# Performance work log

Hardware: AMD Instinct MI355X
Metric: run time of the kernel (lower is better)

## Reference

```python
import jax, jax.numpy as jnp
import numpy as np


def _graph_conv_mean(x, src, dst, edge_weight, W_rel, W_root, b, num_nodes):
    # messages: gather source features, optionally scale by edge weight
    msg = x[src]  # [E, D]
    if edge_weight is not None:
        msg = msg * edge_weight[:, None]
    # mean aggregation over incoming edges per destination node
    summed = jax.ops.segment_sum(msg, dst, num_segments=num_nodes)  # [N, D]
    count = jax.ops.segment_sum(jnp.ones((src.shape[0],), x.dtype), dst, num_segments=num_nodes)
    mean = summed / jnp.maximum(count, 1.0)[:, None]
    # out = lin_rel(mean) + lin_root(x) + bias
    return mean @ W_rel + x @ W_root + b


def setup_inputs() -> dict:
    key = jax.random.key(0)
    ks = jax.random.split(key, 8)
    N, E, D, H, C = 100000, 1600000, 128, 32, 5
    x = jax.random.normal(ks[0], (N, D), dtype=jnp.float32)
    edge_index = jax.random.randint(ks[1], (2, E), 0, N, dtype=jnp.int64)
    edge_weight = jax.random.uniform(ks[2], (E,), dtype=jnp.float32)
    W_rel1 = jax.random.normal(ks[3], (D, H), dtype=jnp.float32) / np.sqrt(D)
    W_root1 = jax.random.normal(ks[4], (D, H), dtype=jnp.float32) / np.sqrt(D)
    b1 = jnp.zeros((H,), jnp.float32)
    W_rel2 = jax.random.normal(ks[5], (H, C), dtype=jnp.float32) / np.sqrt(H)
    W_root2 = jax.random.normal(ks[6], (H, C), dtype=jnp.float32) / np.sqrt(H)
    b2 = jnp.zeros((C,), jnp.float32)
    return {"x": x, "edge_index": edge_index, "edge_weight": edge_weight,
            "W_rel1": W_rel1, "W_root1": W_root1, "b1": b1,
            "W_rel2": W_rel2, "W_root2": W_root2, "b2": b2}


def reference(x, edge_index, edge_weight, W_rel1, W_root1, b1, W_rel2, W_root2, b2):
    N = x.shape[0]
    src, dst = edge_index[0], edge_index[1]
    # conv1 with edge_weight
    h = _graph_conv_mean(x, src, dst, edge_weight, W_rel1, W_root1, b1, N)
    h = jax.nn.relu(h)
    # dropout is identity at inference (training=False)
    # conv2 without edge_weight
    out = _graph_conv_mean(h, src, dst, None, W_rel2, W_root2, b2, N)
    return jax.nn.log_softmax(out, axis=1)
```

## Files before the change

### kernel.cpp

```cpp
#include <hip/hip_runtime.h>
#include <math.h>

#define N_NODES 100000
#define E_EDGES 1600000
#define D_IN    128
#define H_MID   32
#define C_OUT   5

#define BSHIFT 9
#define BNODES 512
#define NBKT   196
#define BCAP   9200
#define SRC_BITS 17
#define SRC_MASK 0x1FFFF

#define KP 136

typedef __attribute__((ext_vector_type(8))) short bf16x8;
typedef __attribute__((ext_vector_type(4))) float f32x4;

__device__ inline unsigned f2bf(float f) {
    unsigned u = __float_as_uint(f);
    return (u + 0x7FFFu + ((u >> 16) & 1u)) >> 16;
}

__global__ void k_prep(const float* __restrict__ Wrel,
                       const float* __restrict__ Wroot,
                       int* __restrict__ bucket_cursor,
                       unsigned short* __restrict__ wt_g) {
    int tid = threadIdx.x;
    bucket_cursor[tid] = 0;
    for (int i = tid; i < 64 * 128; i += 256) {
        int n = i >> 7, k = i & 127;
        float v = (n < H_MID) ? Wrel[k * H_MID + n] : Wroot[k * H_MID + (n - H_MID)];
        wt_g[i] = (unsigned short)f2bf(v);
    }
}

__global__ __launch_bounds__(256) void k1_mfma(
    const float* __restrict__ x,
    const unsigned short* __restrict__ wt_g,
    const float* __restrict__ b1,
    unsigned short* __restrict__ xrelh,
    float* __restrict__ xroot) {
    __shared__ unsigned short xs[64 * KP];
    int tid = threadIdx.x;
    int nodeBase = blockIdx.x * 64;

    #pragma unroll
    for (int it = 0; it < 16; ++it) {
        int idx = it * 256 + tid;
        int row = idx >> 6, kp = idx & 63;
        int node = nodeBase + row;
        float2 v = make_float2(0.f, 0.f);
        if (node < N_NODES)
            v = *(const float2*)(x + (size_t)node * D_IN + kp * 2);
        unsigned pk = f2bf(v.x) | (f2bf(v.y) << 16);
        *(unsigned*)(xs + row * KP + kp * 2) = pk;
    }
    __syncthreads();

    int lane = tid & 63;
    int wv = tid >> 6;
    int m = lane & 15;
    int quad = lane >> 4;

    f32x4 acc[4];
    #pragma unroll
    for (int nt = 0; nt < 4; ++nt) acc[nt] = (f32x4){0.f, 0.f, 0.f, 0.f};

    #pragma unroll
    for (int kk = 0; kk < 4; ++kk) {
        int k0 = kk * 32 + quad * 8;
        bf16x8 a = *(const bf16x8*)(xs + (wv * 16 + m) * KP + k0);
        #pragma unroll
        for (int nt = 0; nt < 4; ++nt) {
            bf16x8 b = *(const bf16x8*)(wt_g + (nt * 16 + m) * 128 + k0);
            acc[nt] = __builtin_amdgcn_mfma_f32_16x16x32_bf16(a, b, acc[nt], 0, 0, 0);
        }
    }

    #pragma unroll
    for (int nt = 0; nt < 4; ++nt) {
        #pragma unroll
        for (int r = 0; r < 4; ++r) {
            int node = nodeBase + wv * 16 + quad * 4 + r;
            int colg = nt * 16 + m;
            if (node < N_NODES) {
                if (colg < H_MID) {
                    xrelh[(size_t)node * H_MID + colg] =
                        (unsigned short)f2bf(acc[nt][r]);
                } else {
                    int c = colg - H_MID;
                    xroot[(size_t)node * H_MID + c] = acc[nt][r] + b1[c];
                }
            }
        }
    }
}

__global__ __launch_bounds__(1024) void k_binA(
    const int* __restrict__ src,
    const int* __restrict__ dst,
    const float* __restrict__ ew,
    int* __restrict__ bucket_cursor,
    int2* __restrict__ staged) {
    __shared__ int cnt[NBKT];
    __shared__ int lstart[NBKT];
    __shared__ int gbase[NBKT];
    __shared__ int scanbuf[256];
    __shared__ int2 ebuf[2048];
    __shared__ short bbuf[2048];
    int tid = threadIdx.x;
    int eBase = blockIdx.x * 2048;

    if (tid < NBKT) cnt[tid] = 0;
    __syncthreads();

    int b[2], rank[2], packed[2], wbits[2];
    bool valid[2];
    #pragma unroll
    for (int u = 0; u < 2; ++u) {
        int e = eBase + u * 1024 + tid;
        valid[u] = (e < E_EDGES);
        b[u] = 0; rank[u] = 0; packed[u] = 0; wbits[u] = 0;
        if (valid[u]) {
            int d = dst[e];
            int s = src[e];
            wbits[u] = __float_as_int(ew[e]);
            b[u] = d >> BSHIFT;
            packed[u] = ((d & (BNODES - 1)) << SRC_BITS) | s;
            rank[u] = atomicAdd(&cnt[b[u]], 1);
        }
    }
    __syncthreads();

    if (tid < 256) scanbuf[tid] = (tid < NBKT) ? cnt[tid] : 0;
    __syncthreads();
    for (int off = 1; off < 256; off <<= 1) {
        int t = 0;
        if (tid < 256 && tid >= off) t = scanbuf[tid - off];
        __syncthreads();
        if (tid < 256) scanbuf[tid] += t;
        __syncthreads();
    }
    if (tid < NBKT) {
        lstart[tid] = scanbuf[tid] - cnt[tid];
        gbase[tid]  = atomicAdd(&bucket_cursor[tid], cnt[tid]);
    }
    __syncthreads();
    int total = scanbuf[NBKT - 1];

    #pragma unroll
    for (int u = 0; u < 2; ++u) {
        if (valid[u]) {
            int slot = lstart[b[u]] + rank[u];
            ebuf[slot] = make_int2(packed[u], wbits[u]);
            bbuf[slot] = (short)b[u];
        }
    }
    __syncthreads();

    for (int t = tid; t < total; t += 1024) {
        int2 ev = ebuf[t];
        int bb = bbuf[t];
        int gpos = gbase[bb] + (t - lstart[bb]);
        if (gpos < BCAP)
            staged[(size_t)bb * BCAP + gpos] = ev;
    }
}

__global__ __launch_bounds__(1024) void k_binB2(
    const int* __restrict__ bucket_cursor,
    const int2* __restrict__ staged,
    int* __restrict__ deg,
    int* __restrict__ offsets,
    int2* __restrict__ csr8) {
    __shared__ int hist[BNODES];
    __shared__ int scanb[BNODES];
    __shared__ int cur[BNODES];
    __shared__ int sbase[256];
    int tid = threadIdx.x;
    int b = blockIdx.x;

    if (tid < 256) {
        int c = (tid < NBKT) ? bucket_cursor[tid] : 0;
        sbase[tid] = (c > BCAP) ? BCAP : c;
    }
    if (tid < BNODES) hist[tid] = 0;
    __syncthreads();
    for (int off = 1; off < 256; off <<= 1) {
        int t = 0;
        if (tid < 256 && tid >= off) t = sbase[tid - off];
        __syncthreads();
        if (tid < 256) sbase[tid] += t;
        __syncthreads();
    }
    int count = bucket_cursor[b];
    if (count > BCAP) count = BCAP;
    int base = sbase[b] - count;
    int nodeBase = b << BSHIFT;
    const int2* sp = staged + (size_t)b * BCAP;

    for (int i = tid; i < count; i += 1024)
        atomicAdd(&hist[((unsigned)sp[i].x) >> SRC_BITS], 1);
    __syncthreads();

    int v = 0;
    if (tid < BNODES) {
        v = hist[tid];
        scanb[tid] = v;
    }
    __syncthreads();
    for (int off = 1; off < BNODES; off <<= 1) {
        int t = 0;
        if (tid < BNODES && tid >= off) t = scanb[tid - off];
        __syncthreads();
        if (tid < BNODES) scanb[tid] += t;
        __syncthreads();
    }
    if (tid < BNODES) {
        int excl = scanb[tid] - v;
        int node = nodeBase + tid;
        if (node < N_NODES) {
            deg[node]     = v;
            offsets[node] = base + excl;
        }
        cur[tid] = excl;
    }
    __syncthreads();

    for (int i = tid; i < count; i += 1024) {
        int2 ev = sp[i];
        int local = ((unsigned)ev.x) >> SRC_BITS;
        int pos = atomicAdd(&cur[local], 1);
        csr8[base + pos] = make_int2(ev.x & SRC_MASK, ev.y);
    }
}

__global__ __launch_bounds__(512) void k_layer1(
    const int* __restrict__ offsets,
    const int* __restrict__ deg,
    const int2* __restrict__ csr8,
    const unsigned short* __restrict__ xrelh,
    const float* __restrict__ xroot,
    const float* __restrict__ Wrel2,
    const float* __restrict__ Wroot2,
    const float* __restrict__ b2,
    float* __restrict__ h2rel,
    float* __restrict__ h2root) {
    int node = blockIdx.x * 32 + (threadIdx.x >> 4);
    int lane = threadIdx.x & 15;
    int beg = offsets[node];
    int dg  = deg[node];
    int end = beg + dg;

    float acc0 = 0.f, acc1 = 0.f;
    int i = beg;
    for (; i + 8 <= end; i += 8) {
        int2 e[8];
        unsigned v[8];
        #pragma unroll
        for (int u = 0; u < 8; ++u) e[u] = csr8[i + u];
        #pragma unroll
        for (int u = 0; u < 8; ++u)
            v[u] = *(const unsigned*)(xrelh + (size_t)e[u].x * H_MID + lane * 2);
        #pragma unroll
        for (int u = 0; u < 8; ++u) {
            float w = __int_as_float(e[u].y);
            acc0 += __uint_as_float((v[u] & 0xFFFFu) << 16) * w;
            acc1 += __uint_as_float(v[u] & 0xFFFF0000u) * w;
        }
    }
    for (; i < end; ++i) {
        int2 e0 = csr8[i];
        unsigned v0 = *(const unsigned*)(xrelh + (size_t)e0.x * H_MID + lane * 2);
        float w0 = __int_as_float(e0.y);
        acc0 += __uint_as_float((v0 & 0xFFFFu) << 16) * w0;
        acc1 += __uint_as_float(v0 & 0xFFFF0000u) * w0;
    }

    float inv = 1.0f / fmaxf((float)dg, 1.0f);
    float2 rt = *(const float2*)(xroot + (size_t)node * H_MID + lane * 2);
    float h0 = fmaxf(acc0 * inv + rt.x, 0.f);
    float h1 = fmaxf(acc1 * inv + rt.y, 0.f);

    float p[2 * C_OUT];
    #pragma unroll
    for (int j = 0; j < C_OUT; ++j) {
        p[j]         = h0 * Wrel2[(2 * lane) * C_OUT + j]
                     + h1 * Wrel2[(2 * lane + 1) * C_OUT + j];
        p[C_OUT + j] = h0 * Wroot2[(2 * lane) * C_OUT + j]
                     + h1 * Wroot2[(2 * lane + 1) * C_OUT + j];
    }
    #pragma unroll
    for (int mm = 8; mm > 0; mm >>= 1) {
        #pragma unroll
        for (int j = 0; j < 2 * C_OUT; ++j)
            p[j] += __shfl_xor(p[j], mm, 16);
    }
    if (lane == 0) {
        #pragma unroll
        for (int j = 0; j < C_OUT; ++j) {
            h2rel[(size_t)node * C_OUT + j]  = p[j];
            h2root[(size_t)node * C_OUT + j] = p[C_OUT + j] + b2[j];
        }
    }
}

__global__ __launch_bounds__(256) void k_layer2(
    const int* __restrict__ offsets,
    const int* __restrict__ deg,
    const int2* __restrict__ csr8,
    const float* __restrict__ h2rel,
    const float* __restrict__ h2root,
    float* __restrict__ out) {
    int node = blockIdx.x * 32 + (threadIdx.x >> 3);
    int lane = threadIdx.x & 7;
    int beg = offsets[node];
    int dg  = deg[node];
    int end = beg + dg;

    float acc = 0.f;
    if (lane < C_OUT) {
        int i = beg;
        for (; i + 8 <= end; i += 8) {
            int s[8];
            float v[8];
            #pragma unroll
            for (int u = 0; u < 8; ++u) s[u] = csr8[i + u].x;
            #pragma unroll
            for (int u = 0; u < 8; ++u)
                v[u] = h2rel[(size_t)s[u] * C_OUT + lane];
            #pragma unroll
            for (int u = 0; u < 8; ++u) acc += v[u];
        }
        for (; i < end; ++i)
            acc += h2rel[(size_t)csr8[i].x * C_OUT + lane];
    }
    float inv = 1.0f / fmaxf((float)dg, 1.0f);
    float o = (lane < C_OUT)
                  ? acc * inv + h2root[(size_t)node * C_OUT + lane]
                  : -INFINITY;
    float m = o;
    #pragma unroll
    for (int dd = 4; dd > 0; dd >>= 1) m = fmaxf(m, __shfl_xor(m, dd, 8));
    float e = (lane < C_OUT) ? expf(o - m) : 0.f;
    float ssum = e;
    #pragma unroll
    for (int dd = 4; dd > 0; dd >>= 1) ssum += __shfl_xor(ssum, dd, 8);
    float lse = m + logf(ssum);
    if (lane < C_OUT)
        out[(size_t)node * C_OUT + lane] = o - lse;
}

extern "C" void kernel_launch(void* const* d_in, const int* in_sizes, int n_in,
                              void* d_out, int out_size, void* d_ws, size_t ws_size,
                              hipStream_t stream) {
    const float* x      = (const float*)d_in[0];
    const int*   ei     = (const int*)d_in[1];
    const float* ew     = (const float*)d_in[2];
    const float* Wrel1  = (const float*)d_in[3];
    const float* Wroot1 = (const float*)d_in[4];
    const float* b1     = (const float*)d_in[5];
    const float* Wrel2  = (const float*)d_in[6];
    const float* Wroot2 = (const float*)d_in[7];
    const float* b2     = (const float*)d_in[8];
    float* out = (float*)d_out;

    const int* src = ei;
    const int* dst = ei + E_EDGES;

    char* ws = (char*)d_ws;
    int*   deg           = (int*)ws;
    int*   bucket_cursor = deg + N_NODES;
    unsigned short* wt_g = (unsigned short*)(bucket_cursor + 256);
    int*   offsets       = (int*)(wt_g + 64 * 128);
    int2*  csr8          = (int2*)(offsets + N_NODES);
    unsigned short* xrelh = (unsigned short*)(csr8 + E_EDGES);
    float* xroot         = (float*)(xrelh + (size_t)N_NODES * H_MID);
    float* h2rel         = xroot + (size_t)N_NODES * H_MID;
    float* h2root        = h2rel + (size_t)N_NODES * C_OUT;
    int2*  staged        = (int2*)xrelh;

    k_prep<<<1, 256, 0, stream>>>(Wrel1, Wroot1, bucket_cursor, wt_g);

    k_binA<<<(E_EDGES + 2047) / 2048, 1024, 0, stream>>>(src, dst, ew,
                                                         bucket_cursor, staged);
    k_binB2<<<NBKT, 1024, 0, stream>>>(bucket_cursor, staged,
                                       deg, offsets, csr8);

    k1_mfma<<<(N_NODES + 63) / 64, 256, 0, stream>>>(x, wt_g, b1,
                                                     xrelh, xroot);

    k_layer1<<<N_NODES / 32, 512, 0, stream>>>(offsets, deg, csr8,
                                               xrelh, xroot, Wrel2, Wroot2, b2,
                                               h2rel, h2root);

    k_layer2<<<N_NODES / 32, 256, 0, stream>>>(offsets, deg, csr8,
                                               h2rel, h2root, out);
}
```

Before: 224.3 us.

## Split CSR into separate src/weight arrays, smaller buckets, prefetch edge indices in aggregation

```diff
diff --git a/kernel.cpp b/kernel.cpp
--- a/kernel.cpp
+++ b/kernel.cpp
@@ -7,10 +7,10 @@
 #define H_MID   32
 #define C_OUT   5
 
-#define BSHIFT 9
-#define BNODES 512
-#define NBKT   196
-#define BCAP   9200
+#define BSHIFT 8
+#define BNODES 256
+#define NBKT   391
+#define BCAP   4800
 #define SRC_BITS 17
 #define SRC_MASK 0x1FFFF
 
@@ -30,7 +30,7 @@
                        unsigned short* __restrict__ wt_g) {
     int tid = threadIdx.x;
     bucket_cursor[tid] = 0;
-    for (int i = tid; i < 64 * 128; i += 256) {
+    for (int i = tid; i < 64 * 128; i += 512) {
         int n = i >> 7, k = i & 127;
         float v = (n < H_MID) ? Wrel[k * H_MID + n] : Wroot[k * H_MID + (n - H_MID)];
         wt_g[i] = (unsigned short)f2bf(v);
@@ -108,7 +108,7 @@
     __shared__ int cnt[NBKT];
     __shared__ int lstart[NBKT];
     __shared__ int gbase[NBKT];
-    __shared__ int scanbuf[256];
+    __shared__ int scanbuf[512];
     __shared__ int2 ebuf[2048];
     __shared__ short bbuf[2048];
     int tid = threadIdx.x;
@@ -135,13 +135,13 @@
     }
     __syncthreads();
 
-    if (tid < 256) scanbuf[tid] = (tid < NBKT) ? cnt[tid] : 0;
-    __syncthreads();
-    for (int off = 1; off < 256; off <<= 1) {
+    if (tid < 512) scanbuf[tid] = (tid < NBKT) ? cnt[tid] : 0;
+    __syncthreads();
+    for (int off = 1; off < 512; off <<= 1) {
         int t = 0;
-        if (tid < 256 && tid >= off) t = scanbuf[tid - off];
-        __syncthreads();
-        if (tid < 256) scanbuf[tid] += t;
+        if (tid < 512 && tid >= off) t = scanbuf[tid - off];
+        __syncthreads();
+        if (tid < 512) scanbuf[tid] += t;
         __syncthreads();
     }
     if (tid < NBKT) {
@@ -175,25 +175,26 @@
     const int2* __restrict__ staged,
     int* __restrict__ deg,
     int* __restrict__ offsets,
-    int2* __restrict__ csr8) {
+    int* __restrict__ csr_src,
+    int* __restrict__ csr_wi) {
     __shared__ int hist[BNODES];
     __shared__ int scanb[BNODES];
     __shared__ int cur[BNODES];
-    __shared__ int sbase[256];
+    __shared__ int sbase[512];
     int tid = threadIdx.x;
     int b = blockIdx.x;
 
-    if (tid < 256) {
+    if (tid < 512) {
         int c = (tid < NBKT) ? bucket_cursor[tid] : 0;
         sbase[tid] = (c > BCAP) ? BCAP : c;
     }
     if (tid < BNODES) hist[tid] = 0;
     __syncthreads();
-    for (int off = 1; off < 256; off <<= 1) {
+    for (int off = 1; off < 512; off <<= 1) {
         int t = 0;
-        if (tid < 256 && tid >= off) t = sbase[tid - off];
-        __syncthreads();
-        if (tid < 256) sbase[tid] += t;
+        if (tid < 512 && tid >= off) t = sbase[tid - off];
+        __syncthreads();
+        if (tid < 512) sbase[tid] += t;
         __syncthreads();
     }
     int count = bucket_cursor[b];
@@ -233,15 +234,17 @@
     for (int i = tid; i < count; i += 1024) {
         int2 ev = sp[i];
         int local = ((unsigned)ev.x) >> SRC_BITS;
-        int pos = atomicAdd(&cur[local], 1);
-        csr8[base + pos] = make_int2(ev.x & SRC_MASK, ev.y);
-    }
-}
-
-__global__ __launch_bounds__(512) void k_layer1(
+        int pos = base + atomicAdd(&cur[local], 1);
+        csr_src[pos] = ev.x & SRC_MASK;
+        csr_wi[pos]  = ev.y;
+    }
+}
+
+__global__ __launch_bounds__(256) void k_layer1(
     const int* __restrict__ offsets,
     const int* __restrict__ deg,
-    const int2* __restrict__ csr8,
+    const int* __restrict__ csr_src,
+    const float* __restrict__ csr_w,
     const unsigned short* __restrict__ xrelh,
     const float* __restrict__ xroot,
     const float* __restrict__ Wrel2,
@@ -249,7 +252,7 @@
     const float* __restrict__ b2,
     float* __restrict__ h2rel,
     float* __restrict__ h2root) {
-    int node = blockIdx.x * 32 + (threadIdx.x >> 4);
+    int node = blockIdx.x * 16 + (threadIdx.x >> 4);
     int lane = threadIdx.x & 15;
     int beg = offsets[node];
     int dg  = deg[node];
@@ -257,25 +260,43 @@
 
     float acc0 = 0.f, acc1 = 0.f;
     int i = beg;
-    for (; i + 8 <= end; i += 8) {
-        int2 e[8];
+    int nfull = dg >> 3;
+    if (nfull) {
+        int s[8]; float w[8];
+        #pragma unroll
+        for (int u = 0; u < 8; ++u) { s[u] = csr_src[i + u]; w[u] = csr_w[i + u]; }
+        for (int bb = 1; bb < nfull; ++bb) {
+            unsigned v[8];
+            #pragma unroll
+            for (int u = 0; u < 8; ++u)
+                v[u] = *(const unsigned*)(xrelh + (size_t)s[u] * H_MID + lane * 2);
+            int s2[8]; float w2[8];
+            #pragma unroll
+            for (int u = 0; u < 8; ++u) { s2[u] = csr_src[i + 8 + u]; w2[u] = csr_w[i + 8 + u]; }
+            #pragma unroll
+            for (int u = 0; u < 8; ++u) {
+                acc0 += __uint_as_float((v[u] & 0xFFFFu) << 16) * w[u];
+                acc1 += __uint_as_float(v[u] & 0xFFFF0000u) * w[u];
+            }
+            #pragma unroll
+            for (int u = 0; u < 8; ++u) { s[u] = s2[u]; w[u] = w2[u]; }
+            i += 8;
+        }
         unsigned v[8];
         #pragma unroll
-        for (int u = 0; u < 8; ++u) e[u] = csr8[i + u];
-        #pragma unroll
         for (int u = 0; u < 8; ++u)
-            v[u] = *(const unsigned*)(xrelh + (size_t)e[u].x * H_MID + lane * 2);
+            v[u] = *(const unsigned*)(xrelh + (size_t)s[u] * H_MID + lane * 2);
         #pragma unroll
         for (int u = 0; u < 8; ++u) {
-            float w = __int_as_float(e[u].y);
-            acc0 += __uint_as_float((v[u] & 0xFFFFu) << 16) * w;
-            acc1 += __uint_as_float(v[u] & 0xFFFF0000u) * w;
-        }
+            acc0 += __uint_as_float((v[u] & 0xFFFFu) << 16) * w[u];
+            acc1 += __uint_as_float(v[u] & 0xFFFF0000u) * w[u];
+        }
+        i += 8;
     }
     for (; i < end; ++i) {
-        int2 e0 = csr8[i];
-        unsigned v0 = *(const unsigned*)(xrelh + (size_t)e0.x * H_MID + lane * 2);
-        float w0 = __int_as_float(e0.y);
+        int s0 = csr_src[i];
+        float w0 = csr_w[i];
+        unsigned v0 = *(const unsigned*)(xrelh + (size_t)s0 * H_MID + lane * 2);
         acc0 += __uint_as_float((v0 & 0xFFFFu) << 16) * w0;
         acc1 += __uint_as_float(v0 & 0xFFFF0000u) * w0;
     }
@@ -311,7 +332,7 @@
 __global__ __launch_bounds__(256) void k_layer2(
     const int* __restrict__ offsets,
     const int* __restrict__ deg,
-    const int2* __restrict__ csr8,
+    const int* __restrict__ csr_src,
     const float* __restrict__ h2rel,
     const float* __restrict__ h2root,
     float* __restrict__ out) {
@@ -324,19 +345,32 @@
     float acc = 0.f;
     if (lane < C_OUT) {
         int i = beg;
-        for (; i + 8 <= end; i += 8) {
+        int nfull = dg >> 3;
+        if (nfull) {
             int s[8];
-            float v[8];
-            #pragma unroll
-            for (int u = 0; u < 8; ++u) s[u] = csr8[i + u].x;
+            #pragma unroll
+            for (int u = 0; u < 8; ++u) s[u] = csr_src[i + u];
+            for (int bb = 1; bb < nfull; ++bb) {
+                float v[8];
+                #pragma unroll
+                for (int u = 0; u < 8; ++u)
+                    v[u] = h2rel[(size_t)s[u] * C_OUT + lane];
+                int s2[8];
+                #pragma unroll
+                for (int u = 0; u < 8; ++u) s2[u] = csr_src[i + 8 + u];
+                #pragma unroll
+                for (int u = 0; u < 8; ++u) acc += v[u];
+                #pragma unroll
+                for (int u = 0; u < 8; ++u) s[u] = s2[u];
+                i += 8;
+            }
             #pragma unroll
             for (int u = 0; u < 8; ++u)
-                v[u] = h2rel[(size_t)s[u] * C_OUT + lane];
-            #pragma unroll
-            for (int u = 0; u < 8; ++u) acc += v[u];
+                acc += h2rel[(size_t)s[u] * C_OUT + lane];
+            i += 8;
         }
         for (; i < end; ++i)
-            acc += h2rel[(size_t)csr8[i].x * C_OUT + lane];
+            acc += h2rel[(size_t)csr_src[i] * C_OUT + lane];
     }
     float inv = 1.0f / fmaxf((float)dg, 1.0f);
     float o = (lane < C_OUT)
@@ -374,29 +408,31 @@
     char* ws = (char*)d_ws;
     int*   deg           = (int*)ws;
     int*   bucket_cursor = deg + N_NODES;
-    unsigned short* wt_g = (unsigned short*)(bucket_cursor + 256);
+    unsigned short* wt_g = (unsigned short*)(bucket_cursor + 512);
     int*   offsets       = (int*)(wt_g + 64 * 128);
-    int2*  csr8          = (int2*)(offsets + N_NODES);
-    unsigned short* xrelh = (unsigned short*)(csr8 + E_EDGES);
+    int*   csr_src       = offsets + N_NODES;
+    int*   csr_wi        = csr_src + E_EDGES;
+    unsigned short* xrelh = (unsigned short*)(csr_wi + E_EDGES);
     float* xroot         = (float*)(xrelh + (size_t)N_NODES * H_MID);
     float* h2rel         = xroot + (size_t)N_NODES * H_MID;
     float* h2root        = h2rel + (size_t)N_NODES * C_OUT;
     int2*  staged        = (int2*)xrelh;
 
-    k_prep<<<1, 256, 0, stream>>>(Wrel1, Wroot1, bucket_cursor, wt_g);
+    k_prep<<<1, 512, 0, stream>>>(Wrel1, Wroot1, bucket_cursor, wt_g);
 
     k_binA<<<(E_EDGES + 2047) / 2048, 1024, 0, stream>>>(src, dst, ew,
                                                          bucket_cursor, staged);
     k_binB2<<<NBKT, 1024, 0, stream>>>(bucket_cursor, staged,
-                                       deg, offsets, csr8);
+                                       deg, offsets, csr_src, csr_wi);
 
     k1_mfma<<<(N_NODES + 63) / 64, 256, 0, stream>>>(x, wt_g, b1,
                                                      xrelh, xroot);
 
-    k_layer1<<<N_NODES / 32, 512, 0, stream>>>(offsets, deg, csr8,
+    k_layer1<<<N_NODES / 16, 256, 0, stream>>>(offsets, deg, csr_src,
+                                               (const float*)csr_wi,
                                                xrelh, xroot, Wrel2, Wroot2, b2,
                                                h2rel, h2root);
 
-    k_layer2<<<N_NODES / 32, 256, 0, stream>>>(offsets, deg, csr8,
+    k_layer2<<<N_NODES / 32, 256, 0, stream>>>(offsets, deg, csr_src,
                                                h2rel, h2root, out);
 }
```

Measured after the change: 227.1 us. Within noise of the previous version (+1.2%).

## Drop CSR build; aggregate directly from bucketed edges with LDS atomics

Applied to the files above, without the earlier changes.

```diff
diff --git a/kernel.cpp b/kernel.cpp
--- a/kernel.cpp
+++ b/kernel.cpp
@@ -7,14 +7,16 @@
 #define H_MID   32
 #define C_OUT   5
 
-#define BSHIFT 9
-#define BNODES 512
-#define NBKT   196
-#define BCAP   9200
+#define BSHIFT 8
+#define BNODES 256
+#define NBKT   391
+#define BCAP   4500
 #define SRC_BITS 17
 #define SRC_MASK 0x1FFFF
-
-#define KP 136
+#define EB     4096
+
+#define KP   136
+#define ACCP 33
 
 typedef __attribute__((ext_vector_type(8))) short bf16x8;
 typedef __attribute__((ext_vector_type(4))) float f32x4;
@@ -23,6 +25,9 @@
     unsigned u = __float_as_uint(f);
     return (u + 0x7FFFu + ((u >> 16) & 1u)) >> 16;
 }
+
+__device__ inline float bflo(unsigned v) { return __uint_as_float((v & 0xFFFFu) << 16); }
+__device__ inline float bfhi(unsigned v) { return __uint_as_float(v & 0xFFFF0000u); }
 
 __global__ void k_prep(const float* __restrict__ Wrel,
                        const float* __restrict__ Wroot,
@@ -30,7 +35,7 @@
                        unsigned short* __restrict__ wt_g) {
     int tid = threadIdx.x;
     bucket_cursor[tid] = 0;
-    for (int i = tid; i < 64 * 128; i += 256) {
+    for (int i = tid; i < 64 * 128; i += 512) {
         int n = i >> 7, k = i & 127;
         float v = (n < H_MID) ? Wrel[k * H_MID + n] : Wroot[k * H_MID + (n - H_MID)];
         wt_g[i] = (unsigned short)f2bf(v);
@@ -108,19 +113,19 @@
     __shared__ int cnt[NBKT];
     __shared__ int lstart[NBKT];
     __shared__ int gbase[NBKT];
-    __shared__ int scanbuf[256];
-    __shared__ int2 ebuf[2048];
-    __shared__ short bbuf[2048];
+    __shared__ int scanbuf[512];
+    __shared__ int2 ebuf[EB];
+    __shared__ short bbuf[EB];
     int tid = threadIdx.x;
-    int eBase = blockIdx.x * 2048;
+    int eBase = blockIdx.x * EB;
 
     if (tid < NBKT) cnt[tid] = 0;
     __syncthreads();
 
-    int b[2], rank[2], packed[2], wbits[2];
-    bool valid[2];
-    #pragma unroll
-    for (int u = 0; u < 2; ++u) {
+    int b[4], rank[4], packed[4], wbits[4];
+    bool valid[4];
+    #pragma unroll
+    for (int u = 0; u < 4; ++u) {
         int e = eBase + u * 1024 + tid;
         valid[u] = (e < E_EDGES);
         b[u] = 0; rank[u] = 0; packed[u] = 0; wbits[u] = 0;
@@ -135,13 +140,13 @@
     }
     __syncthreads();
 
-    if (tid < 256) scanbuf[tid] = (tid < NBKT) ? cnt[tid] : 0;
-    __syncthreads();
-    for (int off = 1; off < 256; off <<= 1) {
+    if (tid < 512) scanbuf[tid] = (tid < NBKT) ? cnt[tid] : 0;
+    __syncthreads();
+    for (int off = 1; off < 512; off <<= 1) {
         int t = 0;
-        if (tid < 256 && tid >= off) t = scanbuf[tid - off];
+        if (tid < 512 && tid >= off) t = scanbuf[tid - off];
         __syncthreads();
-        if (tid < 256) scanbuf[tid] += t;
+        if (tid < 512) scanbuf[tid] += t;
         __syncthreads();
     }
     if (tid < NBKT) {
@@ -152,7 +157,7 @@
     int total = scanbuf[NBKT - 1];
 
     #pragma unroll
-    for (int u = 0; u < 2; ++u) {
+    for (int u = 0; u < 4; ++u) {
         if (valid[u]) {
             int slot = lstart[b[u]] + rank[u];
             ebuf[slot] = make_int2(packed[u], wbits[u]);
@@ -170,78 +175,9 @@
     }
 }
 
-__global__ __launch_bounds__(1024) void k_binB2(
+__global__ __launch_bounds__(1024) void k_layer1B(
     const int* __restrict__ bucket_cursor,
     const int2* __restrict__ staged,
-    int* __restrict__ deg,
-    int* __restrict__ offsets,
-    int2* __restrict__ csr8) {
-    __shared__ int hist[BNODES];
-    __shared__ int scanb[BNODES];
-    __shared__ int cur[BNODES];
-    __shared__ int sbase[256];
-    int tid = threadIdx.x;
-    int b = blockIdx.x;
-
-    if (tid < 256) {
-        int c = (tid < NBKT) ? bucket_cursor[tid] : 0;
-        sbase[tid] = (c > BCAP) ? BCAP : c;
-    }
-    if (tid < BNODES) hist[tid] = 0;
-    __syncthreads();
-    for (int off = 1; off < 256; off <<= 1) {
-        int t = 0;
-        if (tid < 256 && tid >= off) t = sbase[tid - off];
-        __syncthreads();
-        if (tid < 256) sbase[tid] += t;
-        __syncthreads();
-    }
-    int count = bucket_cursor[b];
-    if (count > BCAP) count = BCAP;
-    int base = sbase[b] - count;
-    int nodeBase = b << BSHIFT;
-    const int2* sp = staged + (size_t)b * BCAP;
-
-    for (int i = tid; i < count; i += 1024)
-        atomicAdd(&hist[((unsigned)sp[i].x) >> SRC_BITS], 1);
-    __syncthreads();
-
-    int v = 0;
-    if (tid < BNODES) {
-        v = hist[tid];
-        scanb[tid] = v;
-    }
-    __syncthreads();
-    for (int off = 1; off < BNODES; off <<= 1) {
-        int t = 0;
-        if (tid < BNODES && tid >= off) t = scanb[tid - off];
-        __syncthreads();
-        if (tid < BNODES) scanb[tid] += t;
-        __syncthreads();
-    }
-    if (tid < BNODES) {
-        int excl = scanb[tid] - v;
-        int node = nodeBase + tid;
-        if (node < N_NODES) {
-            deg[node]     = v;
-            offsets[node] = base + excl;
-        }
-        cur[tid] = excl;
-    }
-    __syncthreads();
-
-    for (int i = tid; i < count; i += 1024) {
-        int2 ev = sp[i];
-        int local = ((unsigned)ev.x) >> SRC_BITS;
-        int pos = atomicAdd(&cur[local], 1);
-        csr8[base + pos] = make_int2(ev.x & SRC_MASK, ev.y);
-    }
-}
-
-__global__ __launch_bounds__(512) void k_layer1(
-    const int* __restrict__ offsets,
-    const int* __restrict__ deg,
-    const int2* __restrict__ csr8,
     const unsigned short* __restrict__ xrelh,
     const float* __restrict__ xroot,
     const float* __restrict__ Wrel2,
@@ -249,109 +185,182 @@
     const float* __restrict__ b2,
     float* __restrict__ h2rel,
     float* __restrict__ h2root) {
-    int node = blockIdx.x * 32 + (threadIdx.x >> 4);
-    int lane = threadIdx.x & 15;
-    int beg = offsets[node];
-    int dg  = deg[node];
-    int end = beg + dg;
-
-    float acc0 = 0.f, acc1 = 0.f;
-    int i = beg;
-    for (; i + 8 <= end; i += 8) {
-        int2 e[8];
-        unsigned v[8];
-        #pragma unroll
-        for (int u = 0; u < 8; ++u) e[u] = csr8[i + u];
-        #pragma unroll
-        for (int u = 0; u < 8; ++u)
-            v[u] = *(const unsigned*)(xrelh + (size_t)e[u].x * H_MID + lane * 2);
-        #pragma unroll
-        for (int u = 0; u < 8; ++u) {
-            float w = __int_as_float(e[u].y);
-            acc0 += __uint_as_float((v[u] & 0xFFFFu) << 16) * w;
-            acc1 += __uint_as_float(v[u] & 0xFFFF0000u) * w;
-        }
-    }
-    for (; i < end; ++i) {
-        int2 e0 = csr8[i];
-        unsigned v0 = *(const unsigned*)(xrelh + (size_t)e0.x * H_MID + lane * 2);
+    __shared__ float acc[BNODES * ACCP];
+    __shared__ int hist[BNODES];
+    int tid = threadIdx.x;
+    int b = blockIdx.x;
+
+    for (int i = tid; i < BNODES * ACCP; i += 1024) acc[i] = 0.f;
+    if (tid < BNODES) hist[tid] = 0;
+    __syncthreads();
+
+    int count = bucket_cursor[b];
+    if (count > BCAP) count = BCAP;
+    const int2* sp = staged + (size_t)b * BCAP;
+
+    int g = tid >> 4;
+    int lane = tid & 15;
+
+    int nb = count >> 8;
+    for (int r = 0; r < nb; ++r) {
+        int i = (r << 8) + (g << 2);
+        int2 e0 = sp[i], e1 = sp[i + 1], e2 = sp[i + 2], e3 = sp[i + 3];
+        unsigned v0 = *(const unsigned*)(xrelh + (size_t)(e0.x & SRC_MASK) * H_MID + lane * 2);
+        unsigned v1 = *(const unsigned*)(xrelh + (size_t)(e1.x & SRC_MASK) * H_MID + lane * 2);
+        unsigned v2 = *(const unsigned*)(xrelh + (size_t)(e2.x & SRC_MASK) * H_MID + lane * 2);
+        unsigned v3 = *(const unsigned*)(xrelh + (size_t)(e3.x & SRC_MASK) * H_MID + lane * 2);
+        int d0 = ((unsigned)e0.x) >> SRC_BITS;
+        int d1 = ((unsigned)e1.x) >> SRC_BITS;
+        int d2 = ((unsigned)e2.x) >> SRC_BITS;
+        int d3 = ((unsigned)e3.x) >> SRC_BITS;
         float w0 = __int_as_float(e0.y);
-        acc0 += __uint_as_float((v0 & 0xFFFFu) << 16) * w0;
-        acc1 += __uint_as_float(v0 & 0xFFFF0000u) * w0;
-    }
-
-    float inv = 1.0f / fmaxf((float)dg, 1.0f);
-    float2 rt = *(const float2*)(xroot + (size_t)node * H_MID + lane * 2);
-    float h0 = fmaxf(acc0 * inv + rt.x, 0.f);
-    float h1 = fmaxf(acc1 * inv + rt.y, 0.f);
-
-    float p[2 * C_OUT];
-    #pragma unroll
-    for (int j = 0; j < C_OUT; ++j) {
-        p[j]         = h0 * Wrel2[(2 * lane) * C_OUT + j]
-                     + h1 * Wrel2[(2 * lane + 1) * C_OUT + j];
-        p[C_OUT + j] = h0 * Wroot2[(2 * lane) * C_OUT + j]
-                     + h1 * Wroot2[(2 * lane + 1) * C_OUT + j];
-    }
-    #pragma unroll
-    for (int mm = 8; mm > 0; mm >>= 1) {
-        #pragma unroll
-        for (int j = 0; j < 2 * C_OUT; ++j)
-            p[j] += __shfl_xor(p[j], mm, 16);
-    }
-    if (lane == 0) {
-        #pragma unroll
-        for (int j = 0; j < C_OUT; ++j) {
-            h2rel[(size_t)node * C_OUT + j]  = p[j];
-            h2root[(size_t)node * C_OUT + j] = p[C_OUT + j] + b2[j];
-        }
-    }
-}
-
-__global__ __launch_bounds__(256) void k_layer2(
-    const int* __restrict__ offsets,
-    const int* __restrict__ deg,
-    const int2* __restrict__ csr8,
+        float w1 = __int_as_float(e1.y);
+        float w2 = __int_as_float(e2.y);
+        float w3 = __int_as_float(e3.y);
+        atomicAdd(&acc[d0 * ACCP + 2 * lane],     bflo(v0) * w0);
+        atomicAdd(&acc[d0 * ACCP + 2 * lane + 1], bfhi(v0) * w0);
+        atomicAdd(&acc[d1 * ACCP + 2 * lane],     bflo(v1) * w1);
+        atomicAdd(&acc[d1 * ACCP + 2 * lane + 1], bfhi(v1) * w1);
+        atomicAdd(&acc[d2 * ACCP + 2 * lane],     bflo(v2) * w2);
+        atomicAdd(&acc[d2 * ACCP + 2 * lane + 1], bfhi(v2) * w2);
+        atomicAdd(&acc[d3 * ACCP + 2 * lane],     bflo(v3) * w3);
+        atomicAdd(&acc[d3 * ACCP + 2 * lane + 1], bfhi(v3) * w3);
+        if (lane == 0) {
+            atomicAdd(&hist[d0], 1);
+            atomicAdd(&hist[d1], 1);
+            atomicAdd(&hist[d2], 1);
+            atomicAdd(&hist[d3], 1);
+        }
+    }
+    for (int i = (nb << 8) + g; i < count; i += 64) {
+        int2 e0 = sp[i];
+        unsigned v0 = *(const unsigned*)(xrelh + (size_t)(e0.x & SRC_MASK) * H_MID + lane * 2);
+        int d0 = ((unsigned)e0.x) >> SRC_BITS;
+        float w0 = __int_as_float(e0.y);
+        atomicAdd(&acc[d0 * ACCP + 2 * lane],     bflo(v0) * w0);
+        atomicAdd(&acc[d0 * ACCP + 2 * lane + 1], bfhi(v0) * w0);
+        if (lane == 0) atomicAdd(&hist[d0], 1);
+    }
+    __syncthreads();
+
+    #pragma unroll
+    for (int pass = 0; pass < 4; ++pass) {
+        int nl = pass * 64 + (tid >> 4);
+        int node = b * BNODES + nl;
+        if (node < N_NODES) {
+            int dg = hist[nl];
+            float inv = 1.0f / fmaxf((float)dg, 1.0f);
+            float a0 = acc[nl * ACCP + 2 * lane] * inv;
+            float a1 = acc[nl * ACCP + 2 * lane + 1] * inv;
+            float2 rt = *(const float2*)(xroot + (size_t)node * H_MID + lane * 2);
+            float h0 = fmaxf(a0 + rt.x, 0.f);
+            float h1 = fmaxf(a1 + rt.y, 0.f);
+
+            float p[2 * C_OUT];
+            #pragma unroll
+            for (int j = 0; j < C_OUT; ++j) {
+                p[j]         = h0 * Wrel2[(2 * lane) * C_OUT + j]
+                             + h1 * Wrel2[(2 * lane + 1) * C_OUT + j];
+                p[C_OUT + j] = h0 * Wroot2[(2 * lane) * C_OUT + j]
+                             + h1 * Wroot2[(2 * lane + 1) * C_OUT + j];
+            }
+            #pragma unroll
+            for (int mm = 8; mm > 0; mm >>= 1) {
+                #pragma unroll
+                for (int j = 0; j < 2 * C_OUT; ++j)
+                    p[j] += __shfl_xor(p[j], mm, 16);
+            }
+            if (lane == 0) {
+                #pragma unroll
+                for (int j = 0; j < C_OUT; ++j) {
+                    h2rel[(size_t)node * C_OUT + j]  = p[j];
+                    h2root[(size_t)node * C_OUT + j] = p[C_OUT + j] + b2[j];
+                }
+            }
+        }
+    }
+}
+
+__global__ __launch_bounds__(1024) void k_layer2B(
+    const int* __restrict__ bucket_cursor,
+    const int2* __restrict__ staged,
     const float* __restrict__ h2rel,
     const float* __restrict__ h2root,
     float* __restrict__ out) {
-    int node = blockIdx.x * 32 + (threadIdx.x >> 3);
-    int lane = threadIdx.x & 7;
-    int beg = offsets[node];
-    int dg  = deg[node];
-    int end = beg + dg;
-
-    float acc = 0.f;
-    if (lane < C_OUT) {
-        int i = beg;
-        for (; i + 8 <= end; i += 8) {
-            int s[8];
-            float v[8];
+    __shared__ float acc2[BNODES * 9];
+    __shared__ int hist[BNODES];
+    int tid = threadIdx.x;
+    int b = blockIdx.x;
+
+    for (int i = tid; i < BNODES * 9; i += 1024) acc2[i] = 0.f;
+    if (tid < BNODES) hist[tid] = 0;
+    __syncthreads();
+
+    int count = bucket_cursor[b];
+    if (count > BCAP) count = BCAP;
+    const int2* sp = staged + (size_t)b * BCAP;
+
+    int g = tid >> 3;
+    int lane = tid & 7;
+
+    int nb = count >> 9;
+    for (int r = 0; r < nb; ++r) {
+        int i = (r << 9) + (g << 2);
+        int2 e0 = sp[i], e1 = sp[i + 1], e2 = sp[i + 2], e3 = sp[i + 3];
+        int d0 = ((unsigned)e0.x) >> SRC_BITS;
+        int d1 = ((unsigned)e1.x) >> SRC_BITS;
+        int d2 = ((unsigned)e2.x) >> SRC_BITS;
+        int d3 = ((unsigned)e3.x) >> SRC_BITS;
+        if (lane < C_OUT) {
+            float v0 = h2rel[(size_t)(e0.x & SRC_MASK) * C_OUT + lane];
+            float v1 = h2rel[(size_t)(e1.x & SRC_MASK) * C_OUT + lane];
+            float v2 = h2rel[(size_t)(e2.x & SRC_MASK) * C_OUT + lane];
+            float v3 = h2rel[(size_t)(e3.x & SRC_MASK) * C_OUT + lane];
+            atomicAdd(&acc2[d0 * 9 + lane], v0);
+            atomicAdd(&acc2[d1 * 9 + lane], v1);
+            atomicAdd(&acc2[d2 * 9 + lane], v2);
+            atomicAdd(&acc2[d3 * 9 + lane], v3);
+        }
+        if (lane == 0) {
+            atomicAdd(&hist[d0], 1);
+            atomicAdd(&hist[d1], 1);
+            atomicAdd(&hist[d2], 1);
+            atomicAdd(&hist[d3], 1);
+        }
+    }
+    for (int i = (nb << 9) + g; i < count; i += 128) {
+        int2 e0 = sp[i];
+        int d0 = ((unsigned)e0.x) >> SRC_BITS;
+        if (lane < C_OUT) {
+            float v0 = h2rel[(size_t)(e0.x & SRC_MASK) * C_OUT + lane];
+            atomicAdd(&acc2[d0 * 9 + lane], v0);
+        }
+        if (lane == 0) atomicAdd(&hist[d0], 1);
+    }
+    __syncthreads();
+
+    #pragma unroll
+    for (int pass = 0; pass < 2; ++pass) {
+        int nl = pass * 128 + (tid >> 3);
+        int node = b * BNODES + nl;
+        if (node < N_NODES) {
+            int dg = hist[nl];
+            float inv = 1.0f / fmaxf((float)dg, 1.0f);
+            float o = (lane < C_OUT)
+                          ? acc2[nl * 9 + lane] * inv + h2root[(size_t)node * C_OUT + lane]
+                          : -INFINITY;
+            float m = o;
             #pragma unroll
-            for (int u = 0; u < 8; ++u) s[u] = csr8[i + u].x;
+            for (int dd = 4; dd > 0; dd >>= 1) m = fmaxf(m, __shfl_xor(m, dd, 8));
+            float e = (lane < C_OUT) ? expf(o - m) : 0.f;
+            float ssum = e;
             #pragma unroll
-            for (int u = 0; u < 8; ++u)
-                v[u] = h2rel[(size_t)s[u] * C_OUT + lane];
-            #pragma unroll
-            for (int u = 0; u < 8; ++u) acc += v[u];
-        }
-        for (; i < end; ++i)
-            acc += h2rel[(size_t)csr8[i].x * C_OUT + lane];
-    }
-    float inv = 1.0f / fmaxf((float)dg, 1.0f);
-    float o = (lane < C_OUT)
-                  ? acc * inv + h2root[(size_t)node * C_OUT + lane]
-                  : -INFINITY;
-    float m = o;
-    #pragma unroll
-    for (int dd = 4; dd > 0; dd >>= 1) m = fmaxf(m, __shfl_xor(m, dd, 8));
-    float e = (lane < C_OUT) ? expf(o - m) : 0.f;
-    float ssum = e;
-    #pragma unroll
-    for (int dd = 4; dd > 0; dd >>= 1) ssum += __shfl_xor(ssum, dd, 8);
-    float lse = m + logf(ssum);
-    if (lane < C_OUT)
-        out[(size_t)node * C_OUT + lane] = o - lse;
+            for (int dd = 4; dd > 0; dd >>= 1) ssum += __shfl_xor(ssum, dd, 8);
+            float lse = m + logf(ssum);
+            if (lane < C_OUT)
+                out[(size_t)node * C_OUT + lane] = o - lse;
+        }
+    }
 }
 
 extern "C" void kernel_launch(void* const* d_in, const int* in_sizes, int n_in,
@@ -372,31 +381,26 @@
     const int* dst = ei + E_EDGES;
 
     char* ws = (char*)d_ws;
-    int*   deg           = (int*)ws;
-    int*   bucket_cursor = deg + N_NODES;
-    unsigned short* wt_g = (unsigned short*)(bucket_cursor + 256);
-    int*   offsets       = (int*)(wt_g + 64 * 128);
-    int2*  csr8          = (int2*)(offsets + N_NODES);
-    unsigned short* xrelh = (unsigned short*)(csr8 + E_EDGES);
+    int*   bucket_cursor = (int*)ws;
+    unsigned short* wt_g = (unsigned short*)(bucket_cursor + 512);
+    int2*  staged        = (int2*)(wt_g + 64 * 128);
+    unsigned short* xrelh = (unsigned short*)(staged + (size_t)NBKT * BCAP);
     float* xroot         = (float*)(xrelh + (size_t)N_NODES * H_MID);
     float* h2rel         = xroot + (size_t)N_NODES * H_MID;
     float* h2root        = h2rel + (size_t)N_NODES * C_OUT;
-    int2*  staged        = (int2*)xrelh;
-
-    k_prep<<<1, 256, 0, stream>>>(Wrel1, Wroot1, bucket_cursor, wt_g);
-
-    k_binA<<<(E_EDGES + 2047) / 2048, 1024, 0, stream>>>(src, dst, ew,
+
+    k_prep<<<1, 512, 0, stream>>>(Wrel1, Wroot1, bucket_cursor, wt_g);
+
+    k_binA<<<(E_EDGES + EB - 1) / EB, 1024, 0, stream>>>(src, dst, ew,
                                                          bucket_cursor, staged);
-    k_binB2<<<NBKT, 1024, 0, stream>>>(bucket_cursor, staged,
-                                       deg, offsets, csr8);
 
     k1_mfma<<<(N_NODES + 63) / 64, 256, 0, stream>>>(x, wt_g, b1,
                                                      xrelh, xroot);
 
-    k_layer1<<<N_NODES / 32, 512, 0, stream>>>(offsets, deg, csr8,
-                                               xrelh, xroot, Wrel2, Wroot2, b2,
-                                               h2rel, h2root);
-
-    k_layer2<<<N_NODES / 32, 256, 0, stream>>>(offsets, deg, csr8,
-                                               h2rel, h2root, out);
-}
+    k_layer1B<<<NBKT, 1024, 0, stream>>>(bucket_cursor, staged,
+                                         xrelh, xroot, Wrel2, Wroot2, b2,
+                                         h2rel, h2root);
+
+    k_layer2B<<<NBKT, 1024, 0, stream>>>(bucket_cursor, staged,
+                                         h2rel, h2root, out);
+}
```

Result: slower. 562.5 us (+150.7%).
